# Optimization experiments

Measured on AMD Instinct MI355X. Metric: run time of the kernel, lower is better.

## Reference

```python
import jax, jax.numpy as jnp
import numpy as np

N_QUBITS = 4
DIM = 2 ** N_QUBITS  # 16
N_LAYERS = 3

# PennyLane default.qubit convention: wire 0 is the most-significant bit.

def _cnot_perm(c, t):
    # CNOT is a basis permutation (involution): flip target bit where control bit is 1
    idx = np.arange(DIM)
    cbit = (idx >> (N_QUBITS - 1 - c)) & 1
    return np.where(cbit == 1, idx ^ (1 << (N_QUBITS - 1 - t)), idx)

# BasicEntanglerLayers ring: CNOT(0,1), CNOT(1,2), CNOT(2,3), CNOT(3,0)
CNOT_PERMS = [jnp.asarray(_cnot_perm(q, (q + 1) % N_QUBITS)) for q in range(N_QUBITS)]
# PauliZ sign table: Z_SIGNS[i, q] = +1 if bit q of basis state i is 0 else -1
Z_SIGNS = jnp.asarray(np.array([[1.0 - 2.0 * ((i >> (N_QUBITS - 1 - q)) & 1)
                                 for q in range(N_QUBITS)] for i in range(DIM)], dtype=np.float32))


def _ry(theta):
    # RY(t) = [[cos t/2, -sin t/2], [sin t/2, cos t/2]] ; theta [...] -> [..., 2, 2] complex64
    c, s = jnp.cos(theta / 2), jnp.sin(theta / 2)
    m = jnp.stack([jnp.stack([c, -s], -1), jnp.stack([s, c], -1)], -2)
    return m.astype(jnp.complex64)


def _rx(theta):
    # RX(t) = [[cos t/2, -i sin t/2], [-i sin t/2, cos t/2]]
    c, s = jnp.cos(theta / 2), jnp.sin(theta / 2)
    z = jnp.zeros_like(c)
    real = jnp.stack([jnp.stack([c, z], -1), jnp.stack([z, c], -1)], -2)
    imag = jnp.stack([jnp.stack([z, -s], -1), jnp.stack([-s, z], -1)], -2)
    return (real + 1j * imag).astype(jnp.complex64)


def _apply_1q(state, gate, q, batched):
    # state [B, 16]; gate [B,2,2] (batched) or [2,2]; apply on qubit q
    B = state.shape[0]
    a, b = 2 ** q, 2 ** (N_QUBITS - 1 - q)
    s = state.reshape(B, a, 2, b)
    if batched:
        s = jnp.einsum('bij,bajc->baic', gate, s)
    else:
        s = jnp.einsum('ij,bajc->baic', gate, s)
    return s.reshape(B, DIM)


def _circuit(inputs, weights):
    B = inputs.shape[0]
    state = jnp.zeros((B, DIM), jnp.complex64).at[:, 0].set(1.0)  # |0000>
    ry = _ry(inputs)  # [B, 4, 2, 2] AngleEmbedding (rotation='Y')
    for q in range(N_QUBITS):
        state = _apply_1q(state, ry[:, q], q, batched=True)
    rx = _rx(weights)  # [3, 4, 2, 2] BasicEntanglerLayers (RX per qubit)
    for l in range(N_LAYERS):
        for q in range(N_QUBITS):
            state = _apply_1q(state, rx[l, q], q, batched=False)
        for q in range(N_QUBITS):  # ring of CNOTs
            state = state[:, CNOT_PERMS[q]]
    probs = state.real ** 2 + state.imag ** 2  # [B, 16]
    return probs @ Z_SIGNS  # [B, 4] PauliZ expectations


def setup_inputs() -> dict:
    key = jax.random.key(0)
    k1, k2 = jax.random.split(key)
    B = 1048576
    inputs = jax.random.normal(k1, (B, N_QUBITS), dtype=jnp.float32)
    weights = jax.random.normal(k2, (N_LAYERS, N_QUBITS), dtype=jnp.float32) * 0.05  # random_normal init
    return {"inputs": inputs, "weights": weights}


def reference(inputs, weights):
    return _circuit(inputs, weights)
```

## Files before the change

### kernel.cpp

```cpp
#include <hip/hip_runtime.h>

#define NQ 4
#define DIM 16
#define NL 3
#define EPT 4
#define BLK 256

__global__ __launch_bounds__(BLK) void qlayer_fused(const float* __restrict__ inputs,
                                                    const float* __restrict__ weights,
                                                    float* __restrict__ out, int B) {
    float cw[NL * NQ], sw[NL * NQ];
#pragma unroll
    for (int i = 0; i < NL * NQ; ++i) {
        float t = 0.5f * weights[i];
        cw[i] = __cosf(t);
        sw[i] = __sinf(t);
    }

    const int base = blockIdx.x * (BLK * EPT) + threadIdx.x;

#pragma unroll
    for (int e = 0; e < EPT; ++e) {
        const int b = base + e * BLK;
        if (b >= B) continue;

        float4 in = reinterpret_cast<const float4*>(inputs)[b];
        float ci[NQ], si[NQ];
        {
            float a;
            a = 0.5f * in.x; ci[0] = __cosf(a); si[0] = __sinf(a);
            a = 0.5f * in.y; ci[1] = __cosf(a); si[1] = __sinf(a);
            a = 0.5f * in.z; ci[2] = __cosf(a); si[2] = __sinf(a);
            a = 0.5f * in.w; ci[3] = __cosf(a); si[3] = __sinf(a);
        }

        float f01[4], f23[4];
        f01[0] = ci[0] * ci[1]; f01[1] = ci[0] * si[1];
        f01[2] = si[0] * ci[1]; f01[3] = si[0] * si[1];
        f23[0] = ci[2] * ci[3]; f23[1] = ci[2] * si[3];
        f23[2] = si[2] * ci[3]; f23[3] = si[2] * si[3];

        float re[DIM], im[DIM];
#pragma unroll
        for (int i = 0; i < DIM; ++i) {
            re[i] = f01[i >> 2] * f23[i & 3];
            im[i] = 0.0f;
        }

#pragma unroll
        for (int l = 0; l < NL; ++l) {
#pragma unroll
            for (int q = 0; q < NQ; ++q) {
                const float c = cw[l * NQ + q];
                const float s = sw[l * NQ + q];
                const int tbit = 1 << (3 - q);
#pragma unroll
                for (int i = 0; i < DIM; ++i) {
                    if (!(i & tbit)) {
                        const int j = i | tbit;
                        float r0 = re[i], i0 = im[i];
                        float r1 = re[j], i1 = im[j];
                        re[i] = c * r0 + s * i1;
                        im[i] = c * i0 - s * r1;
                        re[j] = c * r1 + s * i0;
                        im[j] = c * i1 - s * r0;
                    }
                }
            }
#pragma unroll
            for (int q = 0; q < NQ; ++q) {
                const int cbit = 1 << (3 - q);
                const int tbit = 1 << (3 - ((q + 1) % NQ));
                float nr[DIM], ni[DIM];
#pragma unroll
                for (int i = 0; i < DIM; ++i) {
                    const int j = (i & cbit) ? (i ^ tbit) : i;
                    nr[i] = re[j];
                    ni[i] = im[j];
                }
#pragma unroll
                for (int i = 0; i < DIM; ++i) {
                    re[i] = nr[i];
                    im[i] = ni[i];
                }
            }
        }

        float p[DIM];
#pragma unroll
        for (int i = 0; i < DIM; ++i) p[i] = re[i] * re[i] + im[i] * im[i];

        float s1[8], z3 = 0.0f;
#pragma unroll
        for (int k = 0; k < 8; ++k) {
            s1[k] = p[2 * k] + p[2 * k + 1];
            z3 += p[2 * k] - p[2 * k + 1];
        }
        float s2[4], z2 = 0.0f;
#pragma unroll
        for (int k = 0; k < 4; ++k) {
            s2[k] = s1[2 * k] + s1[2 * k + 1];
            z2 += s1[2 * k] - s1[2 * k + 1];
        }
        float z1 = (s2[0] - s2[1]) + (s2[2] - s2[3]);
        float z0 = (s2[0] + s2[1]) - (s2[2] + s2[3]);

        reinterpret_cast<float4*>(out)[b] = make_float4(z0, z1, z2, z3);
    }
}

extern "C" void kernel_launch(void* const* d_in, const int* in_sizes, int n_in,
                              void* d_out, int out_size, void* d_ws, size_t ws_size,
                              hipStream_t stream) {
    const float* inputs  = (const float*)d_in[0];
    const float* weights = (const float*)d_in[1];
    float* out = (float*)d_out;

    const int B = in_sizes[0] / NQ;
    const int grid = (B + BLK * EPT - 1) / (BLK * EPT);

    qlayer_fused<<<grid, BLK, 0, stream>>>(inputs, weights, out, B);
}
```

Baseline: 81.75 us.

## Diagonalize entangler layers in Walsh-Hadamard basis and replace gate sweeps with WHTs

Rewrites the circuit simulation so the fixed RX+CNOT layers become a diagonal phase in the Hadamard basis, computed once per thread from Walsh-transformed weight angles. Each sample then needs a product-state setup, a phase multiply, two 16-point Walsh-Hadamard transforms on re/im, and one on the probabilities to read out the Z expectations. This targets the many per-element butterfly and permutation operations of the gate-by-gate loop. Elements per thread are also raised, which can lower occupancy; correctness depends on the hand-derived phase index mapping.

```diff
diff --git a/kernel.cpp b/kernel.cpp
--- a/kernel.cpp
+++ b/kernel.cpp
@@ -3,18 +3,49 @@
 #define NQ 4
 #define DIM 16
 #define NL 3
-#define EPT 4
+#define EPT 8
 #define BLK 256
 
-__global__ __launch_bounds__(BLK) void qlayer_fused(const float* __restrict__ inputs,
+#define WHT16(a)                                                        \
+    do {                                                                \
+        _Pragma("unroll")                                               \
+        for (int _len = 1; _len < DIM; _len <<= 1) {                    \
+            _Pragma("unroll")                                           \
+            for (int _i = 0; _i < DIM; ++_i) {                          \
+                if (!(_i & _len)) {                                     \
+                    float _x = (a)[_i], _y = (a)[_i + _len];            \
+                    (a)[_i] = _x + _y;                                  \
+                    (a)[_i + _len] = _x - _y;                           \
+                }                                                       \
+            }                                                           \
+        }                                                               \
+    } while (0)
+
+__global__ __launch_bounds__(BLK) void qlayer_walsh(const float* __restrict__ inputs,
                                                     const float* __restrict__ weights,
                                                     float* __restrict__ out, int B) {
-    float cw[NL * NQ], sw[NL * NQ];
+    float L[DIM];
 #pragma unroll
-    for (int i = 0; i < NL * NQ; ++i) {
-        float t = 0.5f * weights[i];
-        cw[i] = __cosf(t);
-        sw[i] = __sinf(t);
+    for (int i = 0; i < DIM; ++i) L[i] = 0.0f;
+    L[8]  = 0.5f * weights[0];
+    L[4]  = 0.5f * weights[1];
+    L[2]  = 0.5f * weights[2];
+    L[1]  = 0.5f * weights[3];
+    L[12] = 0.5f * weights[4];
+    L[6]  = 0.5f * weights[5];
+    L[3]  = 0.5f * weights[6];
+    L[13] = 0.5f * weights[7];
+    L[10] = 0.5f * weights[8];
+    L[5]  = 0.5f * weights[9];
+    L[14] = 0.5f * weights[10];
+    L[7]  = 0.5f * weights[11];
+    WHT16(L);
+
+    float cL[DIM], sL[DIM];
+#pragma unroll
+    for (int i = 0; i < DIM; ++i) {
+        cL[i] = __cosf(L[i]);
+        sL[i] = __sinf(L[i]);
     }
 
     const int base = blockIdx.x * (BLK * EPT) + threadIdx.x;
@@ -25,87 +56,40 @@
         if (b >= B) continue;
 
         float4 in = reinterpret_cast<const float4*>(inputs)[b];
-        float ci[NQ], si[NQ];
+
+        float u[NQ], v[NQ];
         {
-            float a;
-            a = 0.5f * in.x; ci[0] = __cosf(a); si[0] = __sinf(a);
-            a = 0.5f * in.y; ci[1] = __cosf(a); si[1] = __sinf(a);
-            a = 0.5f * in.z; ci[2] = __cosf(a); si[2] = __sinf(a);
-            a = 0.5f * in.w; ci[3] = __cosf(a); si[3] = __sinf(a);
+            float a, c, s;
+            a = 0.5f * in.x; c = __cosf(a); s = __sinf(a); u[0] = c + s; v[0] = c - s;
+            a = 0.5f * in.y; c = __cosf(a); s = __sinf(a); u[1] = c + s; v[1] = c - s;
+            a = 0.5f * in.z; c = __cosf(a); s = __sinf(a); u[2] = c + s; v[2] = c - s;
+            a = 0.5f * in.w; c = __cosf(a); s = __sinf(a); u[3] = c + s; v[3] = c - s;
         }
 
         float f01[4], f23[4];
-        f01[0] = ci[0] * ci[1]; f01[1] = ci[0] * si[1];
-        f01[2] = si[0] * ci[1]; f01[3] = si[0] * si[1];
-        f23[0] = ci[2] * ci[3]; f23[1] = ci[2] * si[3];
-        f23[2] = si[2] * ci[3]; f23[3] = si[2] * si[3];
+        f01[0] = u[0] * u[1]; f01[1] = u[0] * v[1];
+        f01[2] = v[0] * u[1]; f01[3] = v[0] * v[1];
+        f23[0] = u[2] * u[3]; f23[1] = u[2] * v[3];
+        f23[2] = v[2] * u[3]; f23[3] = v[2] * v[3];
 
         float re[DIM], im[DIM];
 #pragma unroll
         for (int i = 0; i < DIM; ++i) {
-            re[i] = f01[i >> 2] * f23[i & 3];
-            im[i] = 0.0f;
+            float g = f01[i >> 2] * f23[i & 3];
+            re[i] = g * cL[i];
+            im[i] = -g * sL[i];
         }
-
-#pragma unroll
-        for (int l = 0; l < NL; ++l) {
-#pragma unroll
-            for (int q = 0; q < NQ; ++q) {
-                const float c = cw[l * NQ + q];
-                const float s = sw[l * NQ + q];
-                const int tbit = 1 << (3 - q);
-#pragma unroll
-                for (int i = 0; i < DIM; ++i) {
-                    if (!(i & tbit)) {
-                        const int j = i | tbit;
-                        float r0 = re[i], i0 = im[i];
-                        float r1 = re[j], i1 = im[j];
-                        re[i] = c * r0 + s * i1;
-                        im[i] = c * i0 - s * r1;
-                        re[j] = c * r1 + s * i0;
-                        im[j] = c * i1 - s * r0;
-                    }
-                }
-            }
-#pragma unroll
-            for (int q = 0; q < NQ; ++q) {
-                const int cbit = 1 << (3 - q);
-                const int tbit = 1 << (3 - ((q + 1) % NQ));
-                float nr[DIM], ni[DIM];
-#pragma unroll
-                for (int i = 0; i < DIM; ++i) {
-                    const int j = (i & cbit) ? (i ^ tbit) : i;
-                    nr[i] = re[j];
-                    ni[i] = im[j];
-                }
-#pragma unroll
-                for (int i = 0; i < DIM; ++i) {
-                    re[i] = nr[i];
-                    im[i] = ni[i];
-                }
-            }
-        }
+        WHT16(re);
+        WHT16(im);
 
         float p[DIM];
 #pragma unroll
         for (int i = 0; i < DIM; ++i) p[i] = re[i] * re[i] + im[i] * im[i];
 
-        float s1[8], z3 = 0.0f;
-#pragma unroll
-        for (int k = 0; k < 8; ++k) {
-            s1[k] = p[2 * k] + p[2 * k + 1];
-            z3 += p[2 * k] - p[2 * k + 1];
-        }
-        float s2[4], z2 = 0.0f;
-#pragma unroll
-        for (int k = 0; k < 4; ++k) {
-            s2[k] = s1[2 * k] + s1[2 * k + 1];
-            z2 += s1[2 * k] - s1[2 * k + 1];
-        }
-        float z1 = (s2[0] - s2[1]) + (s2[2] - s2[3]);
-        float z0 = (s2[0] + s2[1]) - (s2[2] + s2[3]);
-
-        reinterpret_cast<float4*>(out)[b] = make_float4(z0, z1, z2, z3);
+        WHT16(p);
+        const float inv = 1.0f / 256.0f;
+        reinterpret_cast<float4*>(out)[b] =
+            make_float4(p[4] * inv, p[6] * inv, p[3] * inv, p[9] * inv);
     }
 }
 
@@ -119,5 +103,5 @@
     const int B = in_sizes[0] / NQ;
     const int grid = (B + BLK * EPT - 1) / (BLK * EPT);
 
-    qlayer_fused<<<grid, BLK, 0, stream>>>(inputs, weights, out, B);
+    qlayer_walsh<<<grid, BLK, 0, stream>>>(inputs, weights, out, B);
 }
```

After: 79.34 us. 2.9% less time.
